# Performance work log

Hardware: AMD Instinct MI355X
Metric: run time of the kernel (lower is better)

The kernel has to match this reference:

```python
import jax, jax.numpy as jnp
import numpy as np

ALPHA = 0.2
BN_EPS = 1e-5
NEG = -9e15


def make_quaternion_mul(kernel):
    # kernel: [in/4, out]; split columns into quaternion components
    dim = kernel.shape[1] // 4
    r, i, j, k = jnp.split(kernel, 4, axis=1)
    r2 = jnp.concatenate([r, -i, -j, -k], axis=0)
    i2 = jnp.concatenate([i, r, -k, j], axis=0)
    j2 = jnp.concatenate([j, k, r, -i], axis=0)
    k2 = jnp.concatenate([k, -j, i, r], axis=0)
    return jnp.concatenate([r2, i2, j2, k2], axis=1)  # [in, out]


def setup_inputs() -> dict:
    key = jax.random.key(0)
    k1, k2, k3, k4 = jax.random.split(key, 4)
    N, IN, OUT = 8192, 512, 128
    inp = jax.random.normal(k1, (N, IN), dtype=jnp.float32)
    adj = jax.random.randint(k2, (N, N), 0, 2, dtype=jnp.int32)
    # xavier-like init for params
    W = jax.random.normal(k3, (IN // 4, OUT), dtype=jnp.float32) * (1.0 / np.sqrt(IN // 4))
    a = jax.random.normal(k4, (2 * OUT, 1), dtype=jnp.float32) * (1.0 / np.sqrt(2 * OUT))
    bn_gamma = jnp.ones((OUT,), dtype=jnp.float32)
    bn_beta = jnp.zeros((OUT,), dtype=jnp.float32)
    return {"input": inp, "adj": adj, "W": W, "a": a, "bn_gamma": bn_gamma, "bn_beta": bn_beta}


def reference(input, adj, W, a, bn_gamma, bn_beta):
    out_features = W.shape[1]
    hamilton = make_quaternion_mul(W)           # [in, out]
    h = input @ hamilton                        # [N, out]
    # a_input[i,j] = concat(h_i, h_j); a_input @ a decomposes as
    # (h @ a1)_i + (h @ a2)_j with a1 = a[:out], a2 = a[out:]
    a1 = a[:out_features, 0]                    # [out]
    a2 = a[out_features:, 0]                    # [out]
    s1 = h @ a1                                 # [N]
    s2 = h @ a2                                 # [N]
    e = s1[:, None] + s2[None, :]               # [N, N]
    e = jnp.where(e > 0, e, ALPHA * e)          # leaky_relu
    attention = jnp.where(adj > 0, e, NEG)
    attention = jax.nn.softmax(attention, axis=1)
    # dropout is identity in inference
    h_prime = attention @ h                     # [N, out]
    # BatchNorm1d (training-mode batch statistics, biased variance)
    mean = jnp.mean(h_prime, axis=0)
    var = jnp.var(h_prime, axis=0)
    h_prime = (h_prime - mean) / jnp.sqrt(var + BN_EPS) * bn_gamma + bn_beta
    # concat=True -> ELU
    return jax.nn.elu(h_prime)
```

## Files before the change

kernel.cpp:

```cpp
#include <hip/hip_runtime.h>
#include <hip/hip_bf16.h>
#include <math.h>

#define N_NODES 8192
#define IN_F    512
#define OUT_F   128
#define LRELU_A 0.2f
#define EPS_BN  1e-5f
#define MSH     40.0f
#define NSPLIT  8
#define JSPAN   (N_NODES / NSPLIT)
#define TILE_I  64
#define HSTR    72
#define ASTR    36

typedef unsigned short u16;
typedef unsigned int   u32;
typedef unsigned long long u64;
typedef __attribute__((ext_vector_type(8))) short  short8;
typedef __attribute__((ext_vector_type(4))) float  floatx4;

__device__ __forceinline__ u16 f2bf_rtn(float x) {
    u32 u = __float_as_uint(x);
    return (u16)((u + 0x7fffu + ((u >> 16) & 1u)) >> 16);
}

__global__ __launch_bounds__(256) void k_pack(const int* __restrict__ adj, u32* __restrict__ mask) {
    const int t = threadIdx.x;
    const int lane = t & 63, wid = t >> 6;
    const int row = blockIdx.x * 4 + wid;
    const int* ap = adj + (size_t)row * N_NODES + lane * 4;
    u32* mp = mask + (size_t)row * 256;
    uint4 cur = *(const uint4*)(ap);
#pragma unroll 4
    for (int g = 0; g < 32; ++g) {
        uint4 nxt = cur;
        if (g + 1 < 32) nxt = *(const uint4*)(ap + (g + 1) * 256);
        u64 b0 = __ballot((int)cur.x > 0);
        u64 b1 = __ballot((int)cur.y > 0);
        u64 b2 = __ballot((int)cur.z > 0);
        u64 b3 = __ballot((int)cur.w > 0);
        if (lane < 4) {
            u64 v = (lane == 0) ? b0 : (lane == 1) ? b1 : (lane == 2) ? b2 : b3;
            *(u64*)(mp + g * 8 + lane * 2) = v;
        }
        cur = nxt;
    }
}

__global__ __launch_bounds__(256) void k_hamT(const float* __restrict__ W, u16* __restrict__ hamT,
                                              float* __restrict__ s1, float* __restrict__ s2,
                                              float* __restrict__ cs, float* __restrict__ cq) {
    const int idx = blockIdx.x * 256 + threadIdx.x;
    if (idx < N_NODES) { s1[idx] = 0.f; s2[idx] = 0.f; }
    if (idx < OUT_F)   { cs[idx] = 0.f; cq[idx] = 0.f; }
    const int c = idx >> 9, k = idx & 511;
    const int b = c >> 5, cc = c & 31, p = k >> 7, q = k & 127;
    const u32 NEGMASK = 0x284Eu;
    const float sg = ((NEGMASK >> (b * 4 + p)) & 1u) ? -1.f : 1.f;
    hamT[idx] = f2bf_rtn(sg * W[q * 128 + (b ^ p) * 32 + cc]);
}

__global__ __launch_bounds__(256) void k_h(const float* __restrict__ inp, const u16* __restrict__ hamT,
                                           const float* __restrict__ a,
                                           u16* __restrict__ hT, float* __restrict__ s1, float* __restrict__ s2) {
    __shared__ float inA[2][64 * ASTR];
    const int t = threadIdx.x;
    const int lane = t & 63, wid = t >> 6;
    const int quad = lane >> 4, n = lane & 15;
    const int i0 = blockIdx.x * 64;
    const int chalf = blockIdx.y;
    const int srow = t >> 2, scol = (t & 3) * 8;

    {
        const float* sp = inp + (size_t)(i0 + srow) * IN_F + scol;
        *(float4*)&inA[0][srow * ASTR + scol]     = *(const float4*)sp;
        *(float4*)&inA[0][srow * ASTR + scol + 4] = *(const float4*)(sp + 4);
    }
    __syncthreads();

    floatx4 acc[4];
#pragma unroll
    for (int ct = 0; ct < 4; ct++) acc[ct] = (floatx4){0.f, 0.f, 0.f, 0.f};

#pragma unroll 2
    for (int kk = 0; kk < 16; ++kk) {
        const int cur = kk & 1;
        float4 f0n, f1n;
        const bool more = (kk + 1 < 16);
        if (more) {
            const float* sp = inp + (size_t)(i0 + srow) * IN_F + (kk + 1) * 32 + scol;
            f0n = *(const float4*)sp;
            f1n = *(const float4*)(sp + 4);
        }
        float4 a0 = *(const float4*)&inA[cur][(wid * 16 + n) * ASTR + quad * 8];
        float4 a1 = *(const float4*)&inA[cur][(wid * 16 + n) * ASTR + quad * 8 + 4];
        union { u32 u[4]; short8 s; } fa;
        fa.u[0] = (u32)f2bf_rtn(a0.x) | ((u32)f2bf_rtn(a0.y) << 16);
        fa.u[1] = (u32)f2bf_rtn(a0.z) | ((u32)f2bf_rtn(a0.w) << 16);
        fa.u[2] = (u32)f2bf_rtn(a1.x) | ((u32)f2bf_rtn(a1.y) << 16);
        fa.u[3] = (u32)f2bf_rtn(a1.z) | ((u32)f2bf_rtn(a1.w) << 16);
#pragma unroll
        for (int ct = 0; ct < 4; ++ct) {
            short8 fb = *(const short8*)&hamT[(chalf * 64 + ct * 16 + n) * IN_F + kk * 32 + quad * 8];
            acc[ct] = __builtin_amdgcn_mfma_f32_16x16x32_bf16(fa.s, fb, acc[ct], 0, 0, 0);
        }
        if (more) {
            *(float4*)&inA[cur ^ 1][srow * ASTR + scol]     = f0n;
            *(float4*)&inA[cur ^ 1][srow * ASTR + scol + 4] = f1n;
        }
        __syncthreads();
    }

    const int iw = i0 + wid * 16;
#pragma unroll
    for (int ct = 0; ct < 4; ++ct) {
        const int c = chalf * 64 + ct * 16 + n;
        u64 pk = (u64)f2bf_rtn(acc[ct][0])
               | ((u64)f2bf_rtn(acc[ct][1]) << 16)
               | ((u64)f2bf_rtn(acc[ct][2]) << 32)
               | ((u64)f2bf_rtn(acc[ct][3]) << 48);
        *(u64*)&hT[(size_t)c * N_NODES + iw + quad * 4] = pk;
    }

    float p1[4] = {0.f, 0.f, 0.f, 0.f}, p2[4] = {0.f, 0.f, 0.f, 0.f};
#pragma unroll
    for (int ct = 0; ct < 4; ++ct) {
        const int c = chalf * 64 + ct * 16 + n;
        const float a1v = a[c], a2v = a[OUT_F + c];
#pragma unroll
        for (int r = 0; r < 4; ++r) { p1[r] += acc[ct][r] * a1v; p2[r] += acc[ct][r] * a2v; }
    }
#pragma unroll
    for (int m = 1; m < 16; m <<= 1) {
#pragma unroll
        for (int r = 0; r < 4; ++r) {
            p1[r] += __shfl_xor(p1[r], m, 64);
            p2[r] += __shfl_xor(p2[r], m, 64);
        }
    }
    if (n == 0) {
#pragma unroll
        for (int r = 0; r < 4; ++r) {
            atomicAdd(&s1[iw + quad * 4 + r], p1[r]);
            atomicAdd(&s2[iw + quad * 4 + r], p2[r]);
        }
    }
}

__global__ __launch_bounds__(256, 3) void k_att(const u32* __restrict__ mask, const u16* __restrict__ hT,
                                                const float* __restrict__ s1, const float* __restrict__ s2,
                                                float* __restrict__ Opart, float* __restrict__ Lpart) {
    __shared__ u16 hs[2][128 * HSTR];
    __shared__ float s2s[JSPAN];
    const int t = threadIdx.x;
    const int lane = t & 63, wid = t >> 6;
    const int quad = lane >> 4, n = lane & 15;
    const int i0 = blockIdx.x * TILE_I;
    const int jbase = blockIdx.y * JSPAN;
    const int i_lane = i0 + wid * 16 + n;
    const float s1v = s1[i_lane];
    const int scr = t >> 3, scj = (t & 7) * 8;

    if (t < 256) *(float4*)&s2s[t * 4] = *(const float4*)&s2[jbase + t * 4];

    const u32* mrow = mask + (size_t)i_lane * 256 + (jbase >> 5);
    uint4 mgA = *(const uint4*)(mrow);
    uint4 mgB = *(const uint4*)(mrow + 4);

#pragma unroll
    for (int ps = 0; ps < 4; ++ps) {
        const int cr = ps * 32 + scr;
        uint4 v = *(const uint4*)&hT[(size_t)cr * N_NODES + jbase + scj];
        *(uint4*)&hs[0][cr * HSTR + scj] = v;
    }
    __syncthreads();

    floatx4 acc[8];
#pragma unroll
    for (int ct = 0; ct < 8; ct++) acc[ct] = (floatx4){0.f, 0.f, 0.f, 0.f};
    float Lacc = 0.f;

#pragma unroll 4
    for (int ch = 0; ch < 16; ++ch) {
        const int cur = ch & 1;
        const bool more = (ch + 1 < 16);
        uint4 H[4];
        if (more) {
#pragma unroll
            for (int ps = 0; ps < 4; ++ps) {
                const int cr = ps * 32 + scr;
                H[ps] = *(const uint4*)&hT[(size_t)cr * N_NODES + jbase + (ch + 1) * 64 + scj];
            }
        }
        uint4 mgA_n = mgA, mgB_n = mgB;
        if ((ch & 3) == 3 && more) {
            mgA_n = *(const uint4*)(mrow + ((ch >> 2) + 1) * 8);
            mgB_n = *(const uint4*)(mrow + ((ch >> 2) + 1) * 8 + 4);
        }
        const u32 mg[8] = {mgA.x, mgA.y, mgA.z, mgA.w, mgB.x, mgB.y, mgB.z, mgB.w};

        short8 fa[2];
#pragma unroll
        for (int ks = 0; ks < 2; ++ks) {
            const int jl = ch * 64 + ks * 32 + quad * 8;
            float4 sa = *(const float4*)&s2s[jl];
            float4 sb = *(const float4*)&s2s[jl + 4];
            const float sv[8] = {sa.x, sa.y, sa.z, sa.w, sb.x, sb.y, sb.z, sb.w};
            union { u32 u[4]; short8 s; } cv;
#pragma unroll
            for (int jh = 0; jh < 4; ++jh) {
                float w2[2];
#pragma unroll
                for (int e = 0; e < 2; ++e) {
                    const int jj = jh * 2 + e;
                    const u32 word = mg[(jj & 3) * 2 + ((ch >> 1) & 1)];
                    const int sh = (ch & 1) * 16 + ks * 8 + quad * 2 + (jj >> 2);
                    const u32 mbit = (word >> sh) & 1u;
                    float sc = s1v + sv[jj];
                    sc = fmaxf(sc, LRELU_A * sc);
                    float w = mbit ? __expf(sc - MSH) : 0.f;
                    Lacc += w;
                    w2[e] = w;
                }
                cv.u[jh] = (u32)f2bf_rtn(w2[0]) | ((u32)f2bf_rtn(w2[1]) << 16);
            }
            fa[ks] = cv.s;
        }
#pragma unroll
        for (int ct = 0; ct < 8; ++ct) {
            const int boff = (ct * 16 + n) * HSTR;
            short8 fb0 = *(const short8*)&hs[cur][boff + quad * 8];
            short8 fb1 = *(const short8*)&hs[cur][boff + 32 + quad * 8];
            acc[ct] = __builtin_amdgcn_mfma_f32_16x16x32_bf16(fa[0], fb0, acc[ct], 0, 0, 0);
            acc[ct] = __builtin_amdgcn_mfma_f32_16x16x32_bf16(fa[1], fb1, acc[ct], 0, 0, 0);
        }
        if (more) {
#pragma unroll
            for (int ps = 0; ps < 4; ++ps) {
                const int cr = ps * 32 + scr;
                *(uint4*)&hs[cur ^ 1][cr * HSTR + scj] = H[ps];
            }
        }
        __syncthreads();
        mgA = mgA_n; mgB = mgB_n;
    }

    Lacc += __shfl_xor(Lacc, 16, 64);
    Lacc += __shfl_xor(Lacc, 32, 64);
    if (lane < 16)
        Lpart[(size_t)blockIdx.y * N_NODES + i_lane] = Lacc;

    const size_t obase = (size_t)blockIdx.y * N_NODES * OUT_F;
#pragma unroll
    for (int ct = 0; ct < 8; ++ct) {
#pragma unroll
        for (int r = 0; r < 4; ++r) {
            const int i = i0 + wid * 16 + quad * 4 + r;
            Opart[obase + (size_t)i * OUT_F + ct * 16 + n] = acc[ct][r];
        }
    }
}

__global__ __launch_bounds__(256) void k_comb(const float* __restrict__ Opart, const float* __restrict__ Lpart,
                                              float* __restrict__ hp, float* __restrict__ cs, float* __restrict__ cq) {
    const int t = threadIdx.x;
    const int c = t & 127, half = t >> 7;
    const int ibase = blockIdx.x * 16;
    float sv = 0.f, sq = 0.f;
    for (int k = 0; k < 8; k++) {
        const int i = ibase + half + (k << 1);
        float o = 0.f, L = 0.f;
#pragma unroll
        for (int s = 0; s < NSPLIT; s++) {
            o += Opart[((size_t)s * N_NODES + i) * OUT_F + c];
            L += Lpart[(size_t)s * N_NODES + i];
        }
        float v = L > 0.f ? o / L : 0.f;
        hp[(size_t)i * OUT_F + c] = v;
        sv += v; sq += v * v;
    }
    __shared__ float red[256];
    red[t] = sv; __syncthreads();
    if (half == 0) atomicAdd(&cs[c], sv + red[t + 128]);
    __syncthreads(); red[t] = sq; __syncthreads();
    if (half == 0) atomicAdd(&cq[c], sq + red[t + 128]);
}

__global__ __launch_bounds__(256) void k_bn(const float* __restrict__ hp, const float* __restrict__ cs,
                                            const float* __restrict__ cq, const float* __restrict__ gamma,
                                            const float* __restrict__ beta, float* __restrict__ out) {
    const int idx = blockIdx.x * 256 + threadIdx.x;
    const int c = idx & 127;
    const float mean = cs[c] * (1.f / N_NODES);
    const float var  = cq[c] * (1.f / N_NODES) - mean * mean;
    float x = (hp[idx] - mean) * rsqrtf(var + EPS_BN) * gamma[c] + beta[c];
    x = x > 0.f ? x : expm1f(x);
    out[idx] = x;
}

extern "C" void kernel_launch(void* const* d_in, const int* in_sizes, int n_in,
                              void* d_out, int out_size, void* d_ws, size_t ws_size,
                              hipStream_t stream) {
    (void)in_sizes; (void)n_in; (void)out_size; (void)ws_size;
    const float* inp   = (const float*)d_in[0];
    const int*   adj   = (const int*)d_in[1];
    const float* W     = (const float*)d_in[2];
    const float* a     = (const float*)d_in[3];
    const float* gamma = (const float*)d_in[4];
    const float* beta  = (const float*)d_in[5];
    float* out = (float*)d_out;

    char* wsb = (char*)d_ws;
    u16*   hamT = (u16*)wsb;   wsb += (size_t)OUT_F * IN_F * 2;
    u16*   hT   = (u16*)wsb;   wsb += (size_t)OUT_F * N_NODES * 2;
    float* s1   = (float*)wsb; wsb += N_NODES * 4;
    float* s2   = (float*)wsb; wsb += N_NODES * 4;
    u32*   mask = (u32*)wsb;   wsb += (size_t)N_NODES * 256 * 4;
    float* Op   = (float*)wsb; wsb += (size_t)NSPLIT * N_NODES * OUT_F * 4;
    float* Lp   = (float*)wsb; wsb += (size_t)NSPLIT * N_NODES * 4;
    float* hp   = (float*)wsb; wsb += (size_t)N_NODES * OUT_F * 4;
    float* cs   = (float*)wsb; wsb += OUT_F * 4;
    float* cq   = (float*)wsb; wsb += OUT_F * 4;

    hipLaunchKernelGGL(k_pack, dim3(2048), dim3(256), 0, stream, adj, mask);
    hipLaunchKernelGGL(k_hamT, dim3(256), dim3(256), 0, stream, W, hamT, s1, s2, cs, cq);
    hipLaunchKernelGGL(k_h,    dim3(128, 2), dim3(256), 0, stream, inp, hamT, a, hT, s1, s2);
    hipLaunchKernelGGL(k_att,  dim3(128, NSPLIT), dim3(256), 0, stream, mask, hT, s1, s2, Op, Lp);
    hipLaunchKernelGGL(k_comb, dim3(512), dim3(256), 0, stream, Op, Lp, hp, cs, cq);
    hipLaunchKernelGGL(k_bn,   dim3(4096), dim3(256), 0, stream, hp, cs, cq, gamma, beta, out);
}
```

Measured before the change: 495.3 us.

## Fuse adjacency bitmask packing into attention kernel via shared-memory mask

Removes the separate k_pack kernel and its global bitmask round-trip. Each attention block now reads its own 64-row by 1024-column slice of the int32 adjacency, ballots it into a bitmask in shared memory, and then reads mask words from LDS instead of global memory. This saves one launch plus the mask write and re-read. In exchange it adds more LDS per block, which may reduce occupancy, and puts a heavy serialized prologue load at the start of each attention block.

```diff
diff --git a/kernel.cpp b/kernel.cpp
--- a/kernel.cpp
+++ b/kernel.cpp
@@ -13,6 +13,7 @@
 #define TILE_I  64
 #define HSTR    72
 #define ASTR    36
+#define MSTR    34
 
 typedef unsigned short u16;
 typedef unsigned int   u32;
@@ -23,29 +24,6 @@
 __device__ __forceinline__ u16 f2bf_rtn(float x) {
     u32 u = __float_as_uint(x);
     return (u16)((u + 0x7fffu + ((u >> 16) & 1u)) >> 16);
-}
-
-__global__ __launch_bounds__(256) void k_pack(const int* __restrict__ adj, u32* __restrict__ mask) {
-    const int t = threadIdx.x;
-    const int lane = t & 63, wid = t >> 6;
-    const int row = blockIdx.x * 4 + wid;
-    const int* ap = adj + (size_t)row * N_NODES + lane * 4;
-    u32* mp = mask + (size_t)row * 256;
-    uint4 cur = *(const uint4*)(ap);
-#pragma unroll 4
-    for (int g = 0; g < 32; ++g) {
-        uint4 nxt = cur;
-        if (g + 1 < 32) nxt = *(const uint4*)(ap + (g + 1) * 256);
-        u64 b0 = __ballot((int)cur.x > 0);
-        u64 b1 = __ballot((int)cur.y > 0);
-        u64 b2 = __ballot((int)cur.z > 0);
-        u64 b3 = __ballot((int)cur.w > 0);
-        if (lane < 4) {
-            u64 v = (lane == 0) ? b0 : (lane == 1) ? b1 : (lane == 2) ? b2 : b3;
-            *(u64*)(mp + g * 8 + lane * 2) = v;
-        }
-        cur = nxt;
-    }
 }
 
 __global__ __launch_bounds__(256) void k_hamT(const float* __restrict__ W, u16* __restrict__ hamT,
@@ -148,11 +126,12 @@
     }
 }
 
-__global__ __launch_bounds__(256, 3) void k_att(const u32* __restrict__ mask, const u16* __restrict__ hT,
+__global__ __launch_bounds__(256, 3) void k_att(const int* __restrict__ adj, const u16* __restrict__ hT,
                                                 const float* __restrict__ s1, const float* __restrict__ s2,
                                                 float* __restrict__ Opart, float* __restrict__ Lpart) {
     __shared__ u16 hs[2][128 * HSTR];
     __shared__ float s2s[JSPAN];
+    __shared__ u32 mk[64 * MSTR];
     const int t = threadIdx.x;
     const int lane = t & 63, wid = t >> 6;
     const int quad = lane >> 4, n = lane & 15;
@@ -162,11 +141,36 @@
     const float s1v = s1[i_lane];
     const int scr = t >> 3, scj = (t & 7) * 8;
 
-    if (t < 256) *(float4*)&s2s[t * 4] = *(const float4*)&s2[jbase + t * 4];
-
-    const u32* mrow = mask + (size_t)i_lane * 256 + (jbase >> 5);
-    uint4 mgA = *(const uint4*)(mrow);
-    uint4 mgB = *(const uint4*)(mrow + 4);
+    *(float4*)&s2s[t * 4] = *(const float4*)&s2[jbase + t * 4];
+
+    {
+        const size_t rowbase = (size_t)(i0 + wid * 16);
+#pragma unroll
+        for (int rb = 0; rb < 4; ++rb) {
+            uint4 v[4][4];
+#pragma unroll
+            for (int r = 0; r < 4; ++r) {
+                const int* ap = adj + (rowbase + rb * 4 + r) * N_NODES + jbase + lane * 4;
+#pragma unroll
+                for (int g = 0; g < 4; ++g) v[r][g] = *(const uint4*)(ap + g * 256);
+            }
+#pragma unroll
+            for (int r = 0; r < 4; ++r) {
+                u32* mp = &mk[(wid * 16 + rb * 4 + r) * MSTR];
+#pragma unroll
+                for (int g = 0; g < 4; ++g) {
+                    u64 c0 = __ballot((int)v[r][g].x > 0);
+                    u64 c1 = __ballot((int)v[r][g].y > 0);
+                    u64 c2 = __ballot((int)v[r][g].z > 0);
+                    u64 c3 = __ballot((int)v[r][g].w > 0);
+                    if (lane < 4) {
+                        u64 val = (lane == 0) ? c0 : (lane == 1) ? c1 : (lane == 2) ? c2 : c3;
+                        *(u64*)&mp[g * 8 + lane * 2] = val;
+                    }
+                }
+            }
+        }
+    }
 
 #pragma unroll
     for (int ps = 0; ps < 4; ++ps) {
@@ -175,6 +179,13 @@
         *(uint4*)&hs[0][cr * HSTR + scj] = v;
     }
     __syncthreads();
+
+    u32 m8[8];
+    {
+        const u32* mp = &mk[(wid * 16 + n) * MSTR];
+#pragma unroll
+        for (int w = 0; w < 8; ++w) m8[w] = mp[w];
+    }
 
     floatx4 acc[8];
 #pragma unroll
@@ -193,12 +204,14 @@
                 H[ps] = *(const uint4*)&hT[(size_t)cr * N_NODES + jbase + (ch + 1) * 64 + scj];
             }
         }
-        uint4 mgA_n = mgA, mgB_n = mgB;
+        u32 m8n[8];
+#pragma unroll
+        for (int w = 0; w < 8; ++w) m8n[w] = m8[w];
         if ((ch & 3) == 3 && more) {
-            mgA_n = *(const uint4*)(mrow + ((ch >> 2) + 1) * 8);
-            mgB_n = *(const uint4*)(mrow + ((ch >> 2) + 1) * 8 + 4);
-        }
-        const u32 mg[8] = {mgA.x, mgA.y, mgA.z, mgA.w, mgB.x, mgB.y, mgB.z, mgB.w};
+            const u32* mp = &mk[(wid * 16 + n) * MSTR + ((ch >> 2) + 1) * 8];
+#pragma unroll
+            for (int w = 0; w < 8; ++w) m8n[w] = mp[w];
+        }
 
         short8 fa[2];
 #pragma unroll
@@ -214,7 +227,7 @@
 #pragma unroll
                 for (int e = 0; e < 2; ++e) {
                     const int jj = jh * 2 + e;
-                    const u32 word = mg[(jj & 3) * 2 + ((ch >> 1) & 1)];
+                    const u32 word = m8[(jj & 3) * 2 + ((ch >> 1) & 1)];
                     const int sh = (ch & 1) * 16 + ks * 8 + quad * 2 + (jj >> 2);
                     const u32 mbit = (word >> sh) & 1u;
                     float sc = s1v + sv[jj];
@@ -243,7 +256,8 @@
             }
         }
         __syncthreads();
-        mgA = mgA_n; mgB = mgB_n;
+#pragma unroll
+        for (int w = 0; w < 8; ++w) m8[w] = m8n[w];
     }
 
     Lacc += __shfl_xor(Lacc, 16, 64);
@@ -316,17 +330,15 @@
     u16*   hT   = (u16*)wsb;   wsb += (size_t)OUT_F * N_NODES * 2;
     float* s1   = (float*)wsb; wsb += N_NODES * 4;
     float* s2   = (float*)wsb; wsb += N_NODES * 4;
-    u32*   mask = (u32*)wsb;   wsb += (size_t)N_NODES * 256 * 4;
     float* Op   = (float*)wsb; wsb += (size_t)NSPLIT * N_NODES * OUT_F * 4;
     float* Lp   = (float*)wsb; wsb += (size_t)NSPLIT * N_NODES * 4;
     float* hp   = (float*)wsb; wsb += (size_t)N_NODES * OUT_F * 4;
     float* cs   = (float*)wsb; wsb += OUT_F * 4;
     float* cq   = (float*)wsb; wsb += OUT_F * 4;
 
-    hipLaunchKernelGGL(k_pack, dim3(2048), dim3(256), 0, stream, adj, mask);
     hipLaunchKernelGGL(k_hamT, dim3(256), dim3(256), 0, stream, W, hamT, s1, s2, cs, cq);
     hipLaunchKernelGGL(k_h,    dim3(128, 2), dim3(256), 0, stream, inp, hamT, a, hT, s1, s2);
-    hipLaunchKernelGGL(k_att,  dim3(128, NSPLIT), dim3(256), 0, stream, mask, hT, s1, s2, Op, Lp);
+    hipLaunchKernelGGL(k_att,  dim3(128, NSPLIT), dim3(256), 0, stream, adj, hT, s1, s2, Op, Lp);
     hipLaunchKernelGGL(k_comb, dim3(512), dim3(256), 0, stream, Op, Lp, hp, cs, cq);
     hipLaunchKernelGGL(k_bn,   dim3(4096), dim3(256), 0, stream, hp, cs, cq, gamma, beta, out);
 }
```

After: 483.1 us. 2.5% less time.
